# Kernel tuning notes

Measured on AMD Instinct MI355X. Metric: run time of the kernel, lower is better.

## Reference

```python
import jax, jax.numpy as jnp
import numpy as np

B, N, HID = 32768, 27, 128
SINKHORN_ITERS = 20
LN_EPS = 1e-5


def _layer_norm(x, g, b):
    mu = jnp.mean(x, axis=-1, keepdims=True)
    var = jnp.mean((x - mu) ** 2, axis=-1, keepdims=True)
    return (x - mu) * jax.lax.rsqrt(var + LN_EPS) * g + b


def setup_inputs() -> dict:
    key = jax.random.key(0)
    ks = jax.random.split(key, 6)
    A = jax.random.uniform(ks[0], (B, N, N), dtype=jnp.float32)
    m = jax.random.normal(ks[1], (B, N), dtype=jnp.float32)
    tau_r = jnp.ones((), dtype=jnp.float32)
    # MLP params: LayerNorm(4) -> Linear(4,128) -> ReLU -> Linear(128,128) -> LayerNorm(128)
    ln1_g = jnp.ones((4,), jnp.float32)
    ln1_b = jnp.zeros((4,), jnp.float32)
    W1 = jax.random.normal(ks[2], (4, HID), dtype=jnp.float32) * 0.1
    b1 = jnp.zeros((HID,), jnp.float32)
    W2 = jax.random.normal(ks[3], (HID, HID), dtype=jnp.float32) * 0.05
    b2 = jnp.zeros((HID,), jnp.float32)
    ln2_g = jnp.ones((HID,), jnp.float32)
    ln2_b = jnp.zeros((HID,), jnp.float32)
    protos = jax.random.normal(ks[4], (N, HID), dtype=jnp.float32) * 0.02
    return {"A": A, "m": m, "tau_r": tau_r, "ln1_g": ln1_g, "ln1_b": ln1_b,
            "W1": W1, "b1": b1, "W2": W2, "b2": b2,
            "ln2_g": ln2_g, "ln2_b": ln2_b, "protos": protos}


def reference(A, m, tau_r, ln1_g, ln1_b, W1, b1, W2, b2, ln2_g, ln2_b, protos):
    # ---- feature build: [log1p(rowsum), top1_offdiag, top2_offdiag, m] ----
    row_sum = jnp.sum(A, axis=-1)                       # (B,N)
    eye = jnp.eye(N, dtype=A.dtype)
    offdiag = A * (1.0 - eye)                           # (B,N,N)
    top2_vals, _ = jax.lax.top_k(offdiag, 2)            # (B,N,2)
    feat = jnp.stack([jnp.log1p(row_sum), top2_vals[..., 0], top2_vals[..., 1], m], axis=-1)  # (B,N,4)
    # ---- MLP: LN -> Linear -> ReLU -> (Dropout=id) -> Linear -> LN ----
    h = _layer_norm(feat, ln1_g, ln1_b)
    h = jax.nn.relu(h @ W1 + b1)
    h = h @ W2 + b2
    H = _layer_norm(h, ln2_g, ln2_b)                    # (B,N,HID)
    # ---- scores vs slot prototypes, transposed, temperature ----
    scores = jnp.einsum('bnh,kh->bnk', H, protos)       # (B,N,N)
    log_alpha = jnp.swapaxes(scores, 1, 2) / tau_r
    # ---- log-domain Sinkhorn, 20 iterations ----
    def body(_, la):
        la = la - jax.nn.logsumexp(la, axis=-1, keepdims=True)
        la = la - jax.nn.logsumexp(la, axis=-2, keepdims=True)
        return la
    log_alpha = jax.lax.fori_loop(0, SINKHORN_ITERS, body, log_alpha)
    return jnp.exp(log_alpha)                           # (B,N,N) soft permutation R_L
```

## Files before the change

### kernel.cpp

```cpp
#include <hip/hip_runtime.h>
#include <math.h>

#define NN 27
#define HID 128
#define SITERS 20
#define H1S 136

typedef float    v4    __attribute__((ext_vector_type(4)));
typedef _Float16 f16x8 __attribute__((ext_vector_type(8)));

__global__ void k0_prep(const float* __restrict__ W2, const float* __restrict__ protos,
                        _Float16* __restrict__ Bsw, _Float16* __restrict__ Asw)
{
    int t0 = blockIdx.x * 256 + threadIdx.x;
    for (int idx = t0; idx < 4*8*64*8; idx += 8*256) {
        int j = idx & 7, l = (idx >> 3) & 63, nt = (idx >> 9) & 7, kt = idx >> 12;
        int k = kt*32 + (l >> 4)*8 + j, n = nt*16 + (l & 15);
        Bsw[idx] = (_Float16)W2[k*HID + n];
    }
    for (int idx = t0; idx < 2*4*64*8; idx += 8*256) {
        int j = idx & 7, l = (idx >> 3) & 63, kt = (idx >> 9) & 3, mt = idx >> 11;
        int k = kt*32 + (l >> 4)*8 + j, mm = mt*16 + (l & 15);
        Asw[idx] = (mm < NN) ? (_Float16)protos[mm*HID + k] : (_Float16)0.0f;
    }
}

__global__ __launch_bounds__(64, 4) void k1_mlp(
    const float* __restrict__ A, const float* __restrict__ m,
    const float* __restrict__ tau_r,
    const float* __restrict__ ln1g, const float* __restrict__ ln1b,
    const float* __restrict__ W1, const float* __restrict__ b1,
    const float* __restrict__ b2,
    const float* __restrict__ ln2g, const float* __restrict__ ln2b,
    const _Float16* __restrict__ Bsw, const _Float16* __restrict__ Asw,
    float* __restrict__ out)
{
    __shared__ __align__(16) _Float16 sBuf[32 * H1S];
    __shared__ __align__(16) float    sFeat[NN*4 + 4];

    float*    sA   = (float*)sBuf;
    _Float16* sH1  = sBuf;
    _Float16* sH   = sBuf;

    const int b = blockIdx.x;
    const int l = threadIdx.x;
    const int c = l & 15, g = l >> 4;
    const float* Ab = A + (size_t)b * (NN * NN);

    for (int i = l; i < NN * NN; i += 64) sA[i] = Ab[i];
    __builtin_amdgcn_wave_barrier();

    if (l < NN) {
        const int n = l;
        float sum = 0.f, m1 = -1e30f, m2 = -1e30f;
        #pragma unroll
        for (int j = 0; j < NN; ++j) {
            float a = sA[n * NN + j];
            sum += a;
            float v = (j == n) ? 0.f : a;
            float nm1 = fmaxf(m1, v);
            m2 = fmaxf(m2, fminf(m1, v));
            m1 = nm1;
        }
        float f0 = log1pf(sum), f1 = m1, f2 = m2, f3 = m[(size_t)b * NN + n];
        float mu = 0.25f * (f0 + f1 + f2 + f3);
        float d0 = f0 - mu, d1 = f1 - mu, d2 = f2 - mu, d3 = f3 - mu;
        float var = 0.25f * (d0*d0 + d1*d1 + d2*d2 + d3*d3);
        float rs  = rsqrtf(var + 1e-5f);
        sFeat[n*4 + 0] = d0 * rs * ln1g[0] + ln1b[0];
        sFeat[n*4 + 1] = d1 * rs * ln1g[1] + ln1b[1];
        sFeat[n*4 + 2] = d2 * rs * ln1g[2] + ln1b[2];
        sFeat[n*4 + 3] = d3 * rs * ln1g[3] + ln1b[3];
    }
    __builtin_amdgcn_wave_barrier();

    {
        const float w0a = W1[l],      w1a = W1[HID + l],      w2a = W1[2*HID + l],      w3a = W1[3*HID + l];
        const float w0b = W1[64 + l], w1b = W1[HID + 64 + l], w2b = W1[2*HID + 64 + l], w3b = W1[3*HID + 64 + l];
        const float bba = b1[l], bbb = b1[64 + l];
        #pragma unroll 9
        for (int n = 0; n < NN; ++n) {
            v4 f = *(const v4*)&sFeat[n * 4];
            float va = fmaf(f[0], w0a, fmaf(f[1], w1a, fmaf(f[2], w2a, fmaf(f[3], w3a, bba))));
            float vb = fmaf(f[0], w0b, fmaf(f[1], w1b, fmaf(f[2], w2b, fmaf(f[3], w3b, bbb))));
            sH1[n * H1S + l]      = (_Float16)fmaxf(va, 0.f);
            sH1[n * H1S + 64 + l] = (_Float16)fmaxf(vb, 0.f);
        }
        #pragma unroll
        for (int n = NN; n < 32; ++n) {
            sH1[n * H1S + l]      = (_Float16)0.f;
            sH1[n * H1S + 64 + l] = (_Float16)0.f;
        }
    }
    __builtin_amdgcn_wave_barrier();

    f16x8 af[2][4];
    #pragma unroll
    for (int mt = 0; mt < 2; ++mt)
        #pragma unroll
        for (int kt = 0; kt < 4; ++kt)
            af[mt][kt] = *(const f16x8*)&sH1[(mt*16 + c) * H1S + kt*32 + g*8];

    const f16x8* Bv = (const f16x8*)Bsw;

    float s4[2][4]  = {{0.f,0.f,0.f,0.f},{0.f,0.f,0.f,0.f}};
    float ss4[2][4] = {{0.f,0.f,0.f,0.f},{0.f,0.f,0.f,0.f}};
    #pragma unroll 1
    for (int nt = 0; nt < 8; ++nt) {
        f16x8 bf[4];
        #pragma unroll
        for (int kt = 0; kt < 4; ++kt) bf[kt] = Bv[(kt*8 + nt)*64 + l];
        float b2v = b2[nt*16 + c];
        #pragma unroll
        for (int mt = 0; mt < 2; ++mt) {
            v4 a = (v4)(0.f);
            #pragma unroll
            for (int kt = 0; kt < 4; ++kt)
                a = __builtin_amdgcn_mfma_f32_16x16x32_f16(af[mt][kt], bf[kt], a, 0, 0, 0);
            #pragma unroll
            for (int r = 0; r < 4; ++r) {
                float v = a[r] + b2v;
                s4[mt][r] += v; ss4[mt][r] += v * v;
            }
        }
    }
    float muv[2][4], rsv[2][4];
    #pragma unroll
    for (int mt = 0; mt < 2; ++mt)
        #pragma unroll
        for (int r = 0; r < 4; ++r) {
            #pragma unroll
            for (int mask = 1; mask <= 8; mask <<= 1) {
                s4[mt][r]  += __shfl_xor(s4[mt][r],  mask);
                ss4[mt][r] += __shfl_xor(ss4[mt][r], mask);
            }
            float mu  = s4[mt][r] * (1.0f / HID);
            float var = ss4[mt][r] * (1.0f / HID) - mu * mu;
            muv[mt][r] = mu;
            rsv[mt][r] = rsqrtf(var + 1e-5f);
        }

    #pragma unroll 1
    for (int nt = 0; nt < 8; ++nt) {
        f16x8 bf[4];
        #pragma unroll
        for (int kt = 0; kt < 4; ++kt) bf[kt] = Bv[(kt*8 + nt)*64 + l];
        int col = nt*16 + c;
        float b2v = b2[col], g2 = ln2g[col], bb = ln2b[col];
        #pragma unroll
        for (int mt = 0; mt < 2; ++mt) {
            v4 a = (v4)(0.f);
            #pragma unroll
            for (int kt = 0; kt < 4; ++kt)
                a = __builtin_amdgcn_mfma_f32_16x16x32_f16(af[mt][kt], bf[kt], a, 0, 0, 0);
            #pragma unroll
            for (int r = 0; r < 4; ++r) {
                float hv = (a[r] + b2v - muv[mt][r]) * rsv[mt][r] * g2 + bb;
                sH[(mt*16 + 4*g + r) * H1S + col] = (_Float16)hv;
            }
        }
    }
    __builtin_amdgcn_wave_barrier();

    v4 acc2[2][2];
    acc2[0][0] = (v4)(0.f); acc2[0][1] = (v4)(0.f);
    acc2[1][0] = (v4)(0.f); acc2[1][1] = (v4)(0.f);
    {
        const f16x8* Av = (const f16x8*)Asw;
        #pragma unroll
        for (int kt = 0; kt < 4; ++kt) {
            f16x8 b0  = *(const f16x8*)&sH[(c)      * H1S + kt*32 + g*8];
            f16x8 b1f = *(const f16x8*)&sH[(16 + c) * H1S + kt*32 + g*8];
            f16x8 pa0 = Av[(0*4 + kt)*64 + l];
            f16x8 pa1 = Av[(1*4 + kt)*64 + l];
            acc2[0][0] = __builtin_amdgcn_mfma_f32_16x16x32_f16(pa0, b0,  acc2[0][0], 0, 0, 0);
            acc2[0][1] = __builtin_amdgcn_mfma_f32_16x16x32_f16(pa0, b1f, acc2[0][1], 0, 0, 0);
            acc2[1][0] = __builtin_amdgcn_mfma_f32_16x16x32_f16(pa1, b0,  acc2[1][0], 0, 0, 0);
            acc2[1][1] = __builtin_amdgcn_mfma_f32_16x16x32_f16(pa1, b1f, acc2[1][1], 0, 0, 0);
        }
    }

    float p[2][2][4];
    float rowm1[4], rowp1[4];
    #pragma unroll
    for (int r = 0; r < 4; ++r) {
        rowm1[r] = ((16 + 4*g + r) < NN) ? 1.f : 0.f;
        rowp1[r] = 1.f - rowm1[r];
    }
    const float colm1 = ((16 + c) < NN) ? 1.f : 0.f;
    const float colp1 = 1.f - colm1;
    {
        const float inv_tau = 1.0f / tau_r[0];
        #pragma unroll
        for (int r = 0; r < 4; ++r) {
            p[0][0][r] = __expf(acc2[0][0][r] * inv_tau);
            p[0][1][r] = (colm1 != 0.f) ? __expf(acc2[0][1][r] * inv_tau) : 0.f;
            bool iok = (16 + 4*g + r) < NN;
            p[1][0][r] = iok ? __expf(acc2[1][0][r] * inv_tau) : 0.f;
            p[1][1][r] = (iok && colm1 != 0.f) ? __expf(acc2[1][1][r] * inv_tau) : 0.f;
        }
    }

    for (int it = 0; it < SITERS; ++it) {
        #pragma unroll
        for (int r = 0; r < 4; ++r) {
            float s = p[0][0][r] + p[0][1][r];
            s += __shfl_xor(s, 1);
            s += __shfl_xor(s, 2);
            s += __shfl_xor(s, 4);
            s += __shfl_xor(s, 8);
            float rho = __builtin_amdgcn_rcpf(s);
            p[0][0][r] *= rho;
            p[0][1][r] *= rho;
        }
        #pragma unroll
        for (int r = 0; r < 4; ++r) {
            float s = p[1][0][r] + p[1][1][r];
            s += __shfl_xor(s, 1);
            s += __shfl_xor(s, 2);
            s += __shfl_xor(s, 4);
            s += __shfl_xor(s, 8);
            float rho = __builtin_amdgcn_rcpf(s + rowp1[r]) * rowm1[r];
            p[1][0][r] *= rho;
            p[1][1][r] *= rho;
        }
        float t0 = ((p[0][0][0] + p[0][0][1]) + (p[0][0][2] + p[0][0][3]))
                 + ((p[1][0][0] + p[1][0][1]) + (p[1][0][2] + p[1][0][3]));
        float t1 = ((p[0][1][0] + p[0][1][1]) + (p[0][1][2] + p[0][1][3]))
                 + ((p[1][1][0] + p[1][1][1]) + (p[1][1][2] + p[1][1][3]));
        t0 += __shfl_xor(t0, 16);  t0 += __shfl_xor(t0, 32);
        t1 += __shfl_xor(t1, 16);  t1 += __shfl_xor(t1, 32);
        float rc0 = __builtin_amdgcn_rcpf(t0);
        float rc1 = __builtin_amdgcn_rcpf(t1 + colp1) * colm1;
        #pragma unroll
        for (int mt = 0; mt < 2; ++mt) {
            #pragma unroll
            for (int r = 0; r < 4; ++r) {
                p[mt][0][r] *= rc0;
                p[mt][1][r] *= rc1;
            }
        }
    }

    {
        float* ob = out + (size_t)b * (NN * NN);
        #pragma unroll
        for (int r = 0; r < 4; ++r) {
            int i = 4*g + r;
            ob[i * NN + c] = p[0][0][r];
            if ((16 + c) < NN) ob[i * NN + 16 + c] = p[0][1][r];
        }
        #pragma unroll
        for (int r = 0; r < 4; ++r) {
            int i = 16 + 4*g + r;
            if (i < NN) {
                ob[i * NN + c] = p[1][0][r];
                if ((16 + c) < NN) ob[i * NN + 16 + c] = p[1][1][r];
            }
        }
    }
}

extern "C" void kernel_launch(void* const* d_in, const int* in_sizes, int n_in,
                              void* d_out, int out_size, void* d_ws, size_t ws_size,
                              hipStream_t stream) {
    const float* A      = (const float*)d_in[0];
    const float* m      = (const float*)d_in[1];
    const float* tau_r  = (const float*)d_in[2];
    const float* ln1g   = (const float*)d_in[3];
    const float* ln1b   = (const float*)d_in[4];
    const float* W1     = (const float*)d_in[5];
    const float* b1     = (const float*)d_in[6];
    const float* W2     = (const float*)d_in[7];
    const float* b2     = (const float*)d_in[8];
    const float* ln2g   = (const float*)d_in[9];
    const float* ln2b   = (const float*)d_in[10];
    const float* protos = (const float*)d_in[11];
    float* out = (float*)d_out;

    const int B = in_sizes[0] / (NN * NN);

    _Float16* Bsw = (_Float16*)d_ws;
    _Float16* Asw = (_Float16*)((char*)d_ws + 32768);

    k0_prep<<<8, 256, 0, stream>>>(W2, protos, Bsw, Asw);
    k1_mlp<<<B, 64, 0, stream>>>(A, m, tau_r, ln1g, ln1b, W1, b1, b2,
                                 ln2g, ln2b, Bsw, Asw, out);
}
```

Measured before the change: 514.0 us.

## Shrink LDS footprint, compute layer-1 directly into MFMA registers, pack two batches per block

```diff
diff --git a/kernel.cpp b/kernel.cpp
--- a/kernel.cpp
+++ b/kernel.cpp
@@ -4,7 +4,7 @@
 #define NN 27
 #define HID 128
 #define SITERS 20
-#define H1S 136
+#define CHS 40
 
 typedef float    v4    __attribute__((ext_vector_type(4)));
 typedef _Float16 f16x8 __attribute__((ext_vector_type(8)));
@@ -25,7 +25,7 @@
     }
 }
 
-__global__ __launch_bounds__(64, 4) void k1_mlp(
+__global__ __launch_bounds__(128, 6) void k1_mlp(
     const float* __restrict__ A, const float* __restrict__ m,
     const float* __restrict__ tau_r,
     const float* __restrict__ ln1g, const float* __restrict__ ln1b,
@@ -33,18 +33,20 @@
     const float* __restrict__ b2,
     const float* __restrict__ ln2g, const float* __restrict__ ln2b,
     const _Float16* __restrict__ Bsw, const _Float16* __restrict__ Asw,
-    float* __restrict__ out)
+    float* __restrict__ out, int Btot)
 {
-    __shared__ __align__(16) _Float16 sBuf[32 * H1S];
-    __shared__ __align__(16) float    sFeat[NN*4 + 4];
-
-    float*    sA   = (float*)sBuf;
-    _Float16* sH1  = sBuf;
-    _Float16* sH   = sBuf;
-
-    const int b = blockIdx.x;
-    const int l = threadIdx.x;
+    __shared__ __align__(16) float sU[2][736];
+    __shared__ __align__(16) float sFeat2[2][132];
+
+    const int tid = threadIdx.x;
+    const int w   = tid >> 6, l = tid & 63;
+    const int b   = blockIdx.x * 2 + w;
+    if (b >= Btot) return;
     const int c = l & 15, g = l >> 4;
+
+    float*    sA    = sU[w];
+    _Float16* chunk = (_Float16*)sU[w];
+    float*    sFeat = sFeat2[w];
     const float* Ab = A + (size_t)b * (NN * NN);
 
     for (int i = l; i < NN * NN; i += 64) sA[i] = Ab[i];
@@ -71,38 +73,50 @@
         sFeat[n*4 + 1] = d1 * rs * ln1g[1] + ln1b[1];
         sFeat[n*4 + 2] = d2 * rs * ln1g[2] + ln1b[2];
         sFeat[n*4 + 3] = d3 * rs * ln1g[3] + ln1b[3];
+    } else if (l < 32) {
+        sFeat[l*4 + 0] = 0.f; sFeat[l*4 + 1] = 0.f;
+        sFeat[l*4 + 2] = 0.f; sFeat[l*4 + 3] = 0.f;
     }
     __builtin_amdgcn_wave_barrier();
 
-    {
-        const float w0a = W1[l],      w1a = W1[HID + l],      w2a = W1[2*HID + l],      w3a = W1[3*HID + l];
-        const float w0b = W1[64 + l], w1b = W1[HID + 64 + l], w2b = W1[2*HID + 64 + l], w3b = W1[3*HID + 64 + l];
-        const float bba = b1[l], bbb = b1[64 + l];
-        #pragma unroll 9
-        for (int n = 0; n < NN; ++n) {
-            v4 f = *(const v4*)&sFeat[n * 4];
-            float va = fmaf(f[0], w0a, fmaf(f[1], w1a, fmaf(f[2], w2a, fmaf(f[3], w3a, bba))));
-            float vb = fmaf(f[0], w0b, fmaf(f[1], w1b, fmaf(f[2], w2b, fmaf(f[3], w3b, bbb))));
-            sH1[n * H1S + l]      = (_Float16)fmaxf(va, 0.f);
-            sH1[n * H1S + 64 + l] = (_Float16)fmaxf(vb, 0.f);
-        }
-        #pragma unroll
-        for (int n = NN; n < 32; ++n) {
-            sH1[n * H1S + l]      = (_Float16)0.f;
-            sH1[n * H1S + 64 + l] = (_Float16)0.f;
-        }
-    }
-    __builtin_amdgcn_wave_barrier();
-
+    v4 fr0 = *(const v4*)&sFeat[(0*16 + c) * 4];
+    v4 fr1 = *(const v4*)&sFeat[(1*16 + c) * 4];
     f16x8 af[2][4];
     #pragma unroll
-    for (int mt = 0; mt < 2; ++mt)
-        #pragma unroll
-        for (int kt = 0; kt < 4; ++kt)
-            af[mt][kt] = *(const f16x8*)&sH1[(mt*16 + c) * H1S + kt*32 + g*8];
+    for (int kt = 0; kt < 4; ++kt) {
+        const int c0 = kt*32 + g*8;
+        v4 bA = *(const v4*)&b1[c0];
+        v4 bB = *(const v4*)&b1[c0 + 4];
+        float h0[8], h1v[8];
+        #pragma unroll
+        for (int j = 0; j < 4; ++j) {
+            h0[j] = bA[j];  h0[4+j] = bB[j];
+            h1v[j] = bA[j]; h1v[4+j] = bB[j];
+        }
+        #pragma unroll
+        for (int q = 3; q >= 0; --q) {
+            v4 wA = *(const v4*)&W1[q*HID + c0];
+            v4 wB = *(const v4*)&W1[q*HID + c0 + 4];
+            float fq0 = fr0[q], fq1 = fr1[q];
+            #pragma unroll
+            for (int j = 0; j < 4; ++j) {
+                h0[j]    = fmaf(fq0, wA[j], h0[j]);
+                h0[4+j]  = fmaf(fq0, wB[j], h0[4+j]);
+                h1v[j]   = fmaf(fq1, wA[j], h1v[j]);
+                h1v[4+j] = fmaf(fq1, wB[j], h1v[4+j]);
+            }
+        }
+        f16x8 v0, v1;
+        #pragma unroll
+        for (int j = 0; j < 8; ++j) {
+            v0[j] = (_Float16)fmaxf(h0[j],  0.f);
+            v1[j] = (_Float16)fmaxf(h1v[j], 0.f);
+        }
+        af[0][kt] = v0;
+        af[1][kt] = v1;
+    }
 
     const f16x8* Bv = (const f16x8*)Bsw;
-
     float s4[2][4]  = {{0.f,0.f,0.f,0.f},{0.f,0.f,0.f,0.f}};
     float ss4[2][4] = {{0.f,0.f,0.f,0.f},{0.f,0.f,0.f,0.f}};
     #pragma unroll 1
@@ -140,44 +154,43 @@
             rsv[mt][r] = rsqrtf(var + 1e-5f);
         }
 
-    #pragma unroll 1
-    for (int nt = 0; nt < 8; ++nt) {
-        f16x8 bf[4];
-        #pragma unroll
-        for (int kt = 0; kt < 4; ++kt) bf[kt] = Bv[(kt*8 + nt)*64 + l];
-        int col = nt*16 + c;
-        float b2v = b2[col], g2 = ln2g[col], bb = ln2b[col];
-        #pragma unroll
-        for (int mt = 0; mt < 2; ++mt) {
-            v4 a = (v4)(0.f);
-            #pragma unroll
-            for (int kt = 0; kt < 4; ++kt)
-                a = __builtin_amdgcn_mfma_f32_16x16x32_f16(af[mt][kt], bf[kt], a, 0, 0, 0);
-            #pragma unroll
-            for (int r = 0; r < 4; ++r) {
-                float hv = (a[r] + b2v - muv[mt][r]) * rsv[mt][r] * g2 + bb;
-                sH[(mt*16 + 4*g + r) * H1S + col] = (_Float16)hv;
-            }
-        }
-    }
-    __builtin_amdgcn_wave_barrier();
-
+    const f16x8* Av = (const f16x8*)Asw;
     v4 acc2[2][2];
     acc2[0][0] = (v4)(0.f); acc2[0][1] = (v4)(0.f);
     acc2[1][0] = (v4)(0.f); acc2[1][1] = (v4)(0.f);
-    {
-        const f16x8* Av = (const f16x8*)Asw;
-        #pragma unroll
-        for (int kt = 0; kt < 4; ++kt) {
-            f16x8 b0  = *(const f16x8*)&sH[(c)      * H1S + kt*32 + g*8];
-            f16x8 b1f = *(const f16x8*)&sH[(16 + c) * H1S + kt*32 + g*8];
-            f16x8 pa0 = Av[(0*4 + kt)*64 + l];
-            f16x8 pa1 = Av[(1*4 + kt)*64 + l];
-            acc2[0][0] = __builtin_amdgcn_mfma_f32_16x16x32_f16(pa0, b0,  acc2[0][0], 0, 0, 0);
-            acc2[0][1] = __builtin_amdgcn_mfma_f32_16x16x32_f16(pa0, b1f, acc2[0][1], 0, 0, 0);
-            acc2[1][0] = __builtin_amdgcn_mfma_f32_16x16x32_f16(pa1, b0,  acc2[1][0], 0, 0, 0);
-            acc2[1][1] = __builtin_amdgcn_mfma_f32_16x16x32_f16(pa1, b1f, acc2[1][1], 0, 0, 0);
-        }
+    #pragma unroll 1
+    for (int kt2 = 0; kt2 < 4; ++kt2) {
+        #pragma unroll
+        for (int h = 0; h < 2; ++h) {
+            int nt = kt2*2 + h;
+            f16x8 bf[4];
+            #pragma unroll
+            for (int kt = 0; kt < 4; ++kt) bf[kt] = Bv[(kt*8 + nt)*64 + l];
+            int col = nt*16 + c;
+            float b2v = b2[col], g2 = ln2g[col], bb = ln2b[col];
+            #pragma unroll
+            for (int mt = 0; mt < 2; ++mt) {
+                v4 a = (v4)(0.f);
+                #pragma unroll
+                for (int kt = 0; kt < 4; ++kt)
+                    a = __builtin_amdgcn_mfma_f32_16x16x32_f16(af[mt][kt], bf[kt], a, 0, 0, 0);
+                #pragma unroll
+                for (int r = 0; r < 4; ++r) {
+                    float hv = (a[r] + b2v - muv[mt][r]) * rsv[mt][r] * g2 + bb;
+                    chunk[(mt*16 + 4*g + r) * CHS + h*16 + c] = (_Float16)hv;
+                }
+            }
+        }
+        __builtin_amdgcn_wave_barrier();
+        f16x8 b0  = *(const f16x8*)&chunk[(c)      * CHS + g*8];
+        f16x8 b1f = *(const f16x8*)&chunk[(16 + c) * CHS + g*8];
+        f16x8 pa0 = Av[(0*4 + kt2)*64 + l];
+        f16x8 pa1 = Av[(1*4 + kt2)*64 + l];
+        acc2[0][0] = __builtin_amdgcn_mfma_f32_16x16x32_f16(pa0, b0,  acc2[0][0], 0, 0, 0);
+        acc2[0][1] = __builtin_amdgcn_mfma_f32_16x16x32_f16(pa0, b1f, acc2[0][1], 0, 0, 0);
+        acc2[1][0] = __builtin_amdgcn_mfma_f32_16x16x32_f16(pa1, b0,  acc2[1][0], 0, 0, 0);
+        acc2[1][1] = __builtin_amdgcn_mfma_f32_16x16x32_f16(pa1, b1f, acc2[1][1], 0, 0, 0);
+        __builtin_amdgcn_wave_barrier();
     }
 
     float p[2][2][4];
@@ -284,6 +297,7 @@
     _Float16* Asw = (_Float16*)((char*)d_ws + 32768);
 
     k0_prep<<<8, 256, 0, stream>>>(W2, protos, Bsw, Asw);
-    k1_mlp<<<B, 64, 0, stream>>>(A, m, tau_r, ln1g, ln1b, W1, b1, b2,
-                                 ln2g, ln2b, Bsw, Asw, out);
+    const int blocks1 = (B + 1) / 2;
+    k1_mlp<<<blocks1, 128, 0, stream>>>(A, m, tau_r, ln1g, ln1b, W1, b1, b2,
+                                        ln2g, ln2b, Bsw, Asw, out, B);
 }
```

New measurement: 672.6 us. 30.9% more time.
